# Kernel tuning notes

Hardware: AMD Instinct MI355X
Metric: run time of the kernel (lower is better)

The kernel has to match this reference:

```python
import jax, jax.numpy as jnp
import numpy as np
import math

B, H, N, D = 4, 16, 2048, 64
EPS = 1e-8


def setup_inputs() -> dict:
    key = jax.random.key(0)
    kq, kk, kv = jax.random.split(key, 3)
    Q = jax.random.normal(kq, (B, H, N, D), dtype=jnp.float32)
    K = jax.random.normal(kk, (B, H, N, D), dtype=jnp.float32)
    V = jax.random.normal(kv, (B, H, N, D), dtype=jnp.float32)
    # learnable per-head scale, init g0 = log2(N^2 - N)
    g0 = math.log2(N * N - N)
    qk_scale = jnp.full((H,), g0, dtype=jnp.float32)
    # causal mask, broadcast over (B, H)
    M = jnp.tril(jnp.ones((N, N), dtype=bool))
    return {"Q": Q, "K": K, "V": V, "qk_scale": qk_scale, "M": M}


def reference(Q, K, V, qk_scale, M):
    # L2-normalize Q and K along head dim (cosine attention)
    Q_hat = Q / (jnp.sqrt(jnp.sum(Q * Q, axis=-1, keepdims=True)) + EPS)
    K_hat = K / (jnp.sqrt(jnp.sum(K * K, axis=-1, keepdims=True)) + EPS)
    g = qk_scale[None, :, None, None]  # per-head learnable temperature
    scores = jnp.einsum('bhnd,bhmd->bhnm', Q_hat * g, K_hat)
    scores = jnp.where(M, scores, -jnp.inf)
    attn = jax.nn.softmax(scores, axis=-1)  # stable max-subtract softmax
    return jnp.einsum('bhnm,bhmd->bhnd', attn, V)
```

## Files before the change

kernel.cpp:

```cpp
#include <hip/hip_runtime.h>


#define BATCH 4
#define HEADS 16
#define SEQ   2048
#define DIM   64
#define EPS   1e-8f
#define LOG2E 1.44269504088896340736f

typedef short bf16x8 __attribute__((ext_vector_type(8)));
typedef short s16x4  __attribute__((ext_vector_type(4)));
typedef float fx16   __attribute__((ext_vector_type(16)));
typedef unsigned int u32x4 __attribute__((ext_vector_type(4)));

static __device__ __forceinline__ short f2bf(float x) {
    unsigned u = __float_as_uint(x);
    unsigned r = (u + 0x7fffu + ((u >> 16) & 1u)) >> 16;
    return (short)r;
}
static __device__ __forceinline__ unsigned cvt_pk(float lo, float hi) {
    unsigned r;
    asm("v_cvt_pk_bf16_f32 %0, %1, %2" : "=v"(r) : "v"(lo), "v"(hi));
    return r;
}
static __device__ __forceinline__ void gload_lds16(const short* g, short* l) {
    __builtin_amdgcn_global_load_lds(
        (const __attribute__((address_space(1))) void*)g,
        (__attribute__((address_space(3))) void*)l, 16, 0, 0);
}

#define TLDS 68

__global__ __launch_bounds__(256) void prep_kv(
    const float* __restrict__ K, const float* __restrict__ V,
    short* __restrict__ Kn, short* __restrict__ Vt)
{
    const int nt = blockIdx.x;
    const int bh = blockIdx.y;
    const int tid = threadIdx.x;

    const float* Kb = K + ((size_t)bh * SEQ + (size_t)nt * 64) * DIM;
    short* Kno = Kn + ((size_t)bh << 17) + (nt << 12);
    const int c4 = (tid & 15) * 4;
#pragma unroll
    for (int i = 0; i < 4; ++i) {
        const int r = i * 16 + (tid >> 4);
        float4 v = *(const float4*)(Kb + (size_t)r * DIM + c4);
        float ss = v.x * v.x + v.y * v.y + v.z * v.z + v.w * v.w;
        ss += __shfl_xor(ss, 1);
        ss += __shfl_xor(ss, 2);
        ss += __shfl_xor(ss, 4);
        ss += __shfl_xor(ss, 8);
        float s = 1.0f / (sqrtf(ss) + EPS);
        s16x4 o;
        o[0] = f2bf(v.x * s);
        o[1] = f2bf(v.y * s);
        o[2] = f2bf(v.z * s);
        o[3] = f2bf(v.w * s);
        *(s16x4*)(Kno + (r << 6) + (c4 ^ ((r & 7) << 3))) = o;
    }

    const float* Vb = V + ((size_t)bh * SEQ + (size_t)nt * 64) * DIM;
    short* Vo = Vt + ((size_t)bh << 17) + (nt << 12);
    __shared__ short lds[DIM * TLDS];
    const int cg = tid & 15;
    const int rr = tid >> 4;
#pragma unroll
    for (int i = 0; i < 4; ++i) {
        int n  = rr + i * 16;
        int d0 = cg * 4;
        float4 v = *(const float4*)(Vb + (size_t)n * DIM + d0);
        lds[(d0 + 0) * TLDS + n] = f2bf(v.x);
        lds[(d0 + 1) * TLDS + n] = f2bf(v.y);
        lds[(d0 + 2) * TLDS + n] = f2bf(v.z);
        lds[(d0 + 3) * TLDS + n] = f2bf(v.w);
    }
    __syncthreads();
#pragma unroll
    for (int i = 0; i < 4; ++i) {
        int d  = rr + i * 16;
        int nl = cg * 4;
        s16x4 o;
        o[0] = lds[d * TLDS + nl + 0];
        o[1] = lds[d * TLDS + nl + 1];
        o[2] = lds[d * TLDS + nl + 2];
        o[3] = lds[d * TLDS + nl + 3];
        *(s16x4*)(Vo + (d << 6) + (nl ^ ((d & 7) << 3))) = o;
    }
}

__global__ __launch_bounds__(512) void attn_fwd(
    const float* __restrict__ Q, const float* __restrict__ scale,
    const short* __restrict__ Kn, const short* __restrict__ Vt,
    float* __restrict__ out)
{
    const int lid = blockIdx.x;
    const int bh  = (lid & 7) * 8 + ((lid >> 3) & 7);
    const int qb  = 7 - (lid >> 6);
    const int tid = threadIdx.x;
    const int w   = tid >> 6;
    const int l   = tid & 63;
    const int lq  = l & 31;
    const int hi  = l >> 5;

    const short* Kb = Kn + ((size_t)bh << 17);
    const short* Vb = Vt + ((size_t)bh << 17);
    const float  g  = scale[bh & (HEADS - 1)];

    __shared__ __align__(16) short ldsK[4][64 * 64];
    __shared__ __align__(16) short ldsV[4][64 * 64];

    const int toff = tid * 8;

    const int wlo  = qb * 256 + w * 32;
    const int whi  = wlo + 31;
    const int qrow = wlo + lq;
    const int nkt  = 4 * qb + 4;

    gload_lds16(Kb + toff,        &ldsK[0][toff]);
    gload_lds16(Vb + toff,        &ldsV[0][toff]);
    gload_lds16(Kb + 4096 + toff, &ldsK[1][toff]);
    gload_lds16(Vb + 4096 + toff, &ldsV[1][toff]);

    const float* Qrow = Q + ((size_t)bh * SEQ + qrow) * DIM;
    float qv[4][8];
    float ss = 0.f;
#pragma unroll
    for (int c = 0; c < 4; ++c) {
        float4 a = *(const float4*)(Qrow + c * 16 + hi * 8);
        float4 b = *(const float4*)(Qrow + c * 16 + hi * 8 + 4);
        qv[c][0] = a.x; qv[c][1] = a.y; qv[c][2] = a.z; qv[c][3] = a.w;
        qv[c][4] = b.x; qv[c][5] = b.y; qv[c][6] = b.z; qv[c][7] = b.w;
#pragma unroll
        for (int jj = 0; jj < 8; ++jj) ss += qv[c][jj] * qv[c][jj];
    }
    ss += __shfl_xor(ss, 32);
    const float sc = g * LOG2E / (sqrtf(ss) + EPS);

    bf16x8 qbf[4];
#pragma unroll
    for (int c = 0; c < 4; ++c) {
        u32x4 wds;
#pragma unroll
        for (int m = 0; m < 4; ++m)
            wds[m] = cvt_pk(qv[c][2 * m] * sc, qv[c][2 * m + 1] * sc);
        qbf[c] = __builtin_bit_cast(bf16x8, wds);
    }

    fx16 oacc[2];
#pragma unroll
    for (int dt = 0; dt < 2; ++dt)
#pragma unroll
        for (int r = 0; r < 16; ++r) oacc[dt][r] = 0.f;
    float lsum = 0.f;

    int cur = 0;
    for (int kt = 0; kt < nkt; ++kt) {
        if (kt + 2 < nkt) {
            const int nb = (cur + 2) & 3;
            const short* gK = Kb + (size_t)(kt + 2) * 4096;
            const short* gV = Vb + (size_t)(kt + 2) * 4096;
            gload_lds16(gK + toff, &ldsK[nb][toff]);
            gload_lds16(gV + toff, &ldsV[nb][toff]);
            asm volatile("s_waitcnt vmcnt(4)" ::: "memory");
        } else if (kt + 1 < nkt) {
            asm volatile("s_waitcnt vmcnt(2)" ::: "memory");
        } else {
            asm volatile("s_waitcnt vmcnt(0)" ::: "memory");
        }
        __builtin_amdgcn_s_barrier();

        const int k0 = kt * 64;
        if (k0 <= whi) {
            const short* lk = ldsK[cur];
            const short* lv = ldsV[cur];

            fx16 sacc[2];
#pragma unroll
            for (int t = 0; t < 2; ++t)
#pragma unroll
                for (int r = 0; r < 16; ++r) sacc[t][r] = 0.f;

            bf16x8 kf[2][4];
#pragma unroll
            for (int t = 0; t < 2; ++t)
#pragma unroll
                for (int c = 0; c < 4; ++c) {
                    int r = t * 32 + lq;
                    kf[t][c] = *(const bf16x8*)
                        &lk[(r << 6) + ((c * 16 + hi * 8) ^ ((r & 7) << 3))];
                }
            __builtin_amdgcn_s_setprio(1);
#pragma unroll
            for (int c = 0; c < 4; ++c) {
                sacc[0] = __builtin_amdgcn_mfma_f32_32x32x16_bf16(kf[0][c], qbf[c], sacc[0], 0, 0, 0);
                sacc[1] = __builtin_amdgcn_mfma_f32_32x32x16_bf16(kf[1][c], qbf[c], sacc[1], 0, 0, 0);
            }
            __builtin_amdgcn_s_setprio(0);

            bf16x8 vf[2][4];
#pragma unroll
            for (int dt = 0; dt < 2; ++dt)
#pragma unroll
                for (int ks = 0; ks < 4; ++ks) {
                    int d = dt * 32 + lq;
                    vf[dt][ks] = *(const bf16x8*)
                        &lv[(d << 6) + ((ks * 16 + hi * 8) ^ ((d & 7) << 3))];
                }

            float pv[32];
#pragma unroll
            for (int t = 0; t < 2; ++t)
#pragma unroll
                for (int r = 0; r < 16; ++r) pv[t * 16 + r] = sacc[t][r];

            if (k0 + 63 > wlo) {
#pragma unroll
                for (int t = 0; t < 2; ++t)
#pragma unroll
                    for (int r = 0; r < 16; ++r) {
                        int key = k0 + 32 * t + (r & 3) + 8 * (r >> 2) + 4 * hi;
                        if (key > qrow) pv[t * 16 + r] = -3.0e38f;
                    }
            }

#pragma unroll
            for (int r = 0; r < 32; ++r)
                pv[r] = __builtin_amdgcn_exp2f(pv[r]);

            float ts[16];
#pragma unroll
            for (int r = 0; r < 16; ++r) ts[r] = pv[r] + pv[r + 16];
#pragma unroll
            for (int r = 0; r < 8; ++r) ts[r] += ts[r + 8];
#pragma unroll
            for (int r = 0; r < 4; ++r) ts[r] += ts[r + 4];
            float ps = (ts[0] + ts[1]) + (ts[2] + ts[3]);
            ps += __shfl_xor(ps, 32);
            lsum += ps;

            u32x4 paw[4];
#pragma unroll
            for (int ks = 0; ks < 4; ++ks) {
                const int t = ks >> 1;
                const int b0 = (ks & 1) * 8;
#pragma unroll
                for (int m = 0; m < 2; ++m) {
                    unsigned a = cvt_pk(pv[t * 16 + b0 + 2 * m], pv[t * 16 + b0 + 2 * m + 1]);
                    unsigned b = cvt_pk(pv[t * 16 + b0 + 2 * m + 4], pv[t * 16 + b0 + 2 * m + 5]);
                    asm("v_permlane32_swap_b32 %0, %1" : "+v"(a), "+v"(b));
                    paw[ks][m]     = a;
                    paw[ks][m + 2] = b;
                }
            }

            __builtin_amdgcn_s_setprio(1);
#pragma unroll
            for (int dt = 0; dt < 2; ++dt)
#pragma unroll
                for (int ks = 0; ks < 4; ++ks) {
                    bf16x8 pa = __builtin_bit_cast(bf16x8, paw[ks]);
                    oacc[dt] = __builtin_amdgcn_mfma_f32_32x32x16_bf16(vf[dt][ks], pa, oacc[dt], 0, 0, 0);
                }
            __builtin_amdgcn_s_setprio(0);
        }
        cur = (cur + 1) & 3;
    }

    float inv = 1.0f / lsum;
    size_t rb = ((size_t)bh * SEQ + (size_t)qrow) * DIM;
#pragma unroll
    for (int dt = 0; dt < 2; ++dt)
#pragma unroll
        for (int g4 = 0; g4 < 4; ++g4) {
            float4 o4;
            o4.x = oacc[dt][4 * g4 + 0] * inv;
            o4.y = oacc[dt][4 * g4 + 1] * inv;
            o4.z = oacc[dt][4 * g4 + 2] * inv;
            o4.w = oacc[dt][4 * g4 + 3] * inv;
            *(float4*)(out + rb + dt * 32 + 8 * g4 + 4 * hi) = o4;
        }
}

extern "C" void kernel_launch(void* const* d_in, const int* in_sizes, int n_in,
                              void* d_out, int out_size, void* d_ws, size_t ws_size,
                              hipStream_t stream)
{
    const float* Q  = (const float*)d_in[0];
    const float* K  = (const float*)d_in[1];
    const float* V  = (const float*)d_in[2];
    const float* qs = (const float*)d_in[3];
    float* out = (float*)d_out;

    const size_t nElem = (size_t)BATCH * HEADS * SEQ * DIM;
    short* Kn = (short*)d_ws;
    short* Vt = Kn + nElem;

    {
        dim3 grid(SEQ / 64, BATCH * HEADS);
        prep_kv<<<grid, 256, 0, stream>>>(K, V, Kn, Vt);
    }
    {
        attn_fwd<<<(SEQ / 256) * BATCH * HEADS, 512, 0, stream>>>(Q, qs, Kn, Vt, out);
    }
}
```

Before: 71.05 us.

## Software-pipeline QK^T of the next key tile with softmax of current

The key loop is restructured so that the QK^T MFMAs for tile kt+1 are issued while the exp2, row-sum and bf16 packing of tile kt run. Two score accumulator pairs are ping-ponged through a macro-unrolled loop of two tiles, and a prologue computes the first tile's scores. The prefetch wait tightens from vmcnt(4) to vmcnt(2), because the next tile must already be resident in LDS when its scores are computed early. The aim is to hide the MFMA latency behind VALU softmax work. The cost is higher register pressure from the extra accumulators, which may cut occupancy.

```diff
diff --git a/kernel.cpp b/kernel.cpp
--- a/kernel.cpp
+++ b/kernel.cpp
@@ -154,118 +154,119 @@
         for (int r = 0; r < 16; ++r) oacc[dt][r] = 0.f;
     float lsum = 0.f;
 
-    int cur = 0;
-    for (int kt = 0; kt < nkt; ++kt) {
-        if (kt + 2 < nkt) {
-            const int nb = (cur + 2) & 3;
-            const short* gK = Kb + (size_t)(kt + 2) * 4096;
-            const short* gV = Vb + (size_t)(kt + 2) * 4096;
-            gload_lds16(gK + toff, &ldsK[nb][toff]);
-            gload_lds16(gV + toff, &ldsV[nb][toff]);
-            asm volatile("s_waitcnt vmcnt(4)" ::: "memory");
-        } else if (kt + 1 < nkt) {
-            asm volatile("s_waitcnt vmcnt(2)" ::: "memory");
-        } else {
-            asm volatile("s_waitcnt vmcnt(0)" ::: "memory");
+    asm volatile("s_waitcnt vmcnt(2)" ::: "memory");
+    __builtin_amdgcn_s_barrier();
+
+    fx16 saccA0, saccA1, saccB0, saccB1;
+#pragma unroll
+    for (int r = 0; r < 16; ++r) { saccA0[r] = 0.f; saccA1[r] = 0.f; }
+    {
+        const short* lk = ldsK[0];
+#pragma unroll
+        for (int c = 0; c < 4; ++c) {
+            int r0 = lq, r1 = 32 + lq;
+            bf16x8 k0f = *(const bf16x8*)&lk[(r0 << 6) + ((c * 16 + hi * 8) ^ ((r0 & 7) << 3))];
+            bf16x8 k1f = *(const bf16x8*)&lk[(r1 << 6) + ((c * 16 + hi * 8) ^ ((r1 & 7) << 3))];
+            saccA0 = __builtin_amdgcn_mfma_f32_32x32x16_bf16(k0f, qbf[c], saccA0, 0, 0, 0);
+            saccA1 = __builtin_amdgcn_mfma_f32_32x32x16_bf16(k1f, qbf[c], saccA1, 0, 0, 0);
         }
-        __builtin_amdgcn_s_barrier();
-
-        const int k0 = kt * 64;
-        if (k0 <= whi) {
-            const short* lk = ldsK[cur];
-            const short* lv = ldsV[cur];
-
-            fx16 sacc[2];
-#pragma unroll
-            for (int t = 0; t < 2; ++t)
-#pragma unroll
-                for (int r = 0; r < 16; ++r) sacc[t][r] = 0.f;
-
-            bf16x8 kf[2][4];
-#pragma unroll
-            for (int t = 0; t < 2; ++t)
-#pragma unroll
-                for (int c = 0; c < 4; ++c) {
-                    int r = t * 32 + lq;
-                    kf[t][c] = *(const bf16x8*)
-                        &lk[(r << 6) + ((c * 16 + hi * 8) ^ ((r & 7) << 3))];
-                }
-            __builtin_amdgcn_s_setprio(1);
-#pragma unroll
-            for (int c = 0; c < 4; ++c) {
-                sacc[0] = __builtin_amdgcn_mfma_f32_32x32x16_bf16(kf[0][c], qbf[c], sacc[0], 0, 0, 0);
-                sacc[1] = __builtin_amdgcn_mfma_f32_32x32x16_bf16(kf[1][c], qbf[c], sacc[1], 0, 0, 0);
-            }
-            __builtin_amdgcn_s_setprio(0);
-
-            bf16x8 vf[2][4];
-#pragma unroll
-            for (int dt = 0; dt < 2; ++dt)
-#pragma unroll
-                for (int ks = 0; ks < 4; ++ks) {
-                    int d = dt * 32 + lq;
-                    vf[dt][ks] = *(const bf16x8*)
-                        &lv[(d << 6) + ((ks * 16 + hi * 8) ^ ((d & 7) << 3))];
-                }
-
-            float pv[32];
-#pragma unroll
-            for (int t = 0; t < 2; ++t)
-#pragma unroll
-                for (int r = 0; r < 16; ++r) pv[t * 16 + r] = sacc[t][r];
-
-            if (k0 + 63 > wlo) {
-#pragma unroll
-                for (int t = 0; t < 2; ++t)
-#pragma unroll
-                    for (int r = 0; r < 16; ++r) {
-                        int key = k0 + 32 * t + (r & 3) + 8 * (r >> 2) + 4 * hi;
-                        if (key > qrow) pv[t * 16 + r] = -3.0e38f;
-                    }
-            }
-
-#pragma unroll
-            for (int r = 0; r < 32; ++r)
-                pv[r] = __builtin_amdgcn_exp2f(pv[r]);
-
-            float ts[16];
-#pragma unroll
-            for (int r = 0; r < 16; ++r) ts[r] = pv[r] + pv[r + 16];
-#pragma unroll
-            for (int r = 0; r < 8; ++r) ts[r] += ts[r + 8];
-#pragma unroll
-            for (int r = 0; r < 4; ++r) ts[r] += ts[r + 4];
-            float ps = (ts[0] + ts[1]) + (ts[2] + ts[3]);
-            ps += __shfl_xor(ps, 32);
-            lsum += ps;
-
-            u32x4 paw[4];
-#pragma unroll
-            for (int ks = 0; ks < 4; ++ks) {
-                const int t = ks >> 1;
-                const int b0 = (ks & 1) * 8;
-#pragma unroll
-                for (int m = 0; m < 2; ++m) {
-                    unsigned a = cvt_pk(pv[t * 16 + b0 + 2 * m], pv[t * 16 + b0 + 2 * m + 1]);
-                    unsigned b = cvt_pk(pv[t * 16 + b0 + 2 * m + 4], pv[t * 16 + b0 + 2 * m + 5]);
-                    asm("v_permlane32_swap_b32 %0, %1" : "+v"(a), "+v"(b));
-                    paw[ks][m]     = a;
-                    paw[ks][m + 2] = b;
-                }
-            }
-
-            __builtin_amdgcn_s_setprio(1);
-#pragma unroll
-            for (int dt = 0; dt < 2; ++dt)
-#pragma unroll
-                for (int ks = 0; ks < 4; ++ks) {
-                    bf16x8 pa = __builtin_bit_cast(bf16x8, paw[ks]);
-                    oacc[dt] = __builtin_amdgcn_mfma_f32_32x32x16_bf16(vf[dt][ks], pa, oacc[dt], 0, 0, 0);
-                }
-            __builtin_amdgcn_s_setprio(0);
-        }
-        cur = (cur + 1) & 3;
-    }
+    }
+
+#define TILE_BODY(KT, SC0, SC1, SN0, SN1)                                    \
+    {                                                                        \
+        if ((KT) + 2 < nkt) {                                                \
+            const int nb = ((KT) + 2) & 3;                                   \
+            gload_lds16(Kb + (size_t)((KT) + 2) * 4096 + toff, &ldsK[nb][toff]); \
+            gload_lds16(Vb + (size_t)((KT) + 2) * 4096 + toff, &ldsV[nb][toff]); \
+            asm volatile("s_waitcnt vmcnt(2)" ::: "memory");                 \
+        } else {                                                             \
+            asm volatile("s_waitcnt vmcnt(0)" ::: "memory");                 \
+        }                                                                    \
+        __builtin_amdgcn_s_barrier();                                        \
+        const int k0 = (KT) * 64;                                            \
+        if (k0 <= whi) {                                                     \
+                              \
+            if (k0 + 63 > wlo) {                                             \
+                _Pragma("unroll")                                            \
+                for (int r = 0; r < 16; ++r) {                               \
+                    int key0 = k0 + (r & 3) + 8 * (r >> 2) + 4 * hi;         \
+                    if (key0 > qrow) SC0[r] = -3.0e38f;                      \
+                    if (key0 + 32 > qrow) SC1[r] = -3.0e38f;                 \
+                }                                                            \
+            }                                                                \
+                                                   \
+            _Pragma("unroll")                                                \
+            for (int r = 0; r < 16; ++r) {                                   \
+                SC0[r] = __builtin_amdgcn_exp2f(SC0[r]);                     \
+                SC1[r] = __builtin_amdgcn_exp2f(SC1[r]);                     \
+            }                                                                \
+                    \
+            if ((KT) + 1 < nkt) {                                            \
+                _Pragma("unroll")                                            \
+                for (int r = 0; r < 16; ++r) { SN0[r] = 0.f; SN1[r] = 0.f; } \
+                const short* lkn = ldsK[((KT) + 1) & 3];                     \
+                __builtin_amdgcn_s_setprio(1);                               \
+                _Pragma("unroll")                                            \
+                for (int c = 0; c < 4; ++c) {                                \
+                    int r0 = lq, r1 = 32 + lq;                               \
+                    bf16x8 k0f = *(const bf16x8*)&lkn[(r0 << 6) + ((c * 16 + hi * 8) ^ ((r0 & 7) << 3))]; \
+                    bf16x8 k1f = *(const bf16x8*)&lkn[(r1 << 6) + ((c * 16 + hi * 8) ^ ((r1 & 7) << 3))]; \
+                    SN0 = __builtin_amdgcn_mfma_f32_32x32x16_bf16(k0f, qbf[c], SN0, 0, 0, 0); \
+                    SN1 = __builtin_amdgcn_mfma_f32_32x32x16_bf16(k1f, qbf[c], SN1, 0, 0, 0); \
+                }                                                            \
+                __builtin_amdgcn_s_setprio(0);                               \
+            }                                                                \
+                                                        \
+            float ts[16];                                                    \
+            _Pragma("unroll")                                                \
+            for (int r = 0; r < 16; ++r) ts[r] = SC0[r] + SC1[r];            \
+            _Pragma("unroll")                                                \
+            for (int r = 0; r < 8; ++r) ts[r] += ts[r + 8];                  \
+            _Pragma("unroll")                                                \
+            for (int r = 0; r < 4; ++r) ts[r] += ts[r + 4];                  \
+            float ps = (ts[0] + ts[1]) + (ts[2] + ts[3]);                    \
+            ps += __shfl_xor(ps, 32);                                        \
+            lsum += ps;                                                      \
+                                                    \
+            u32x4 paw[4];                                                    \
+            _Pragma("unroll")                                                \
+            for (int ks = 0; ks < 4; ++ks) {                                 \
+                const int b0 = (ks & 1) * 8;                                 \
+                _Pragma("unroll")                                            \
+                for (int m = 0; m < 2; ++m) {                                \
+                    float xa0 = (ks < 2) ? SC0[b0 + 2 * m]     : SC1[b0 + 2 * m];     \
+                    float xa1 = (ks < 2) ? SC0[b0 + 2 * m + 1] : SC1[b0 + 2 * m + 1]; \
+                    float xb0 = (ks < 2) ? SC0[b0 + 2 * m + 4] : SC1[b0 + 2 * m + 4]; \
+                    float xb1 = (ks < 2) ? SC0[b0 + 2 * m + 5] : SC1[b0 + 2 * m + 5]; \
+                    unsigned a = cvt_pk(xa0, xa1);                           \
+                    unsigned b = cvt_pk(xb0, xb1);                           \
+                    asm("v_permlane32_swap_b32 %0, %1" : "+v"(a), "+v"(b));  \
+                    paw[ks][m]     = a;                                      \
+                    paw[ks][m + 2] = b;                                      \
+                }                                                            \
+            }                                                                \
+                                                           \
+            const short* lv = ldsV[(KT) & 3];                                \
+            __builtin_amdgcn_s_setprio(1);                                   \
+            _Pragma("unroll")                                                \
+            for (int dt = 0; dt < 2; ++dt) {                                 \
+                _Pragma("unroll")                                            \
+                for (int ks = 0; ks < 4; ++ks) {                             \
+                    int d = dt * 32 + lq;                                    \
+                    bf16x8 vf = *(const bf16x8*)&lv[(d << 6) + ((ks * 16 + hi * 8) ^ ((d & 7) << 3))]; \
+                    bf16x8 pa = __builtin_bit_cast(bf16x8, paw[ks]);         \
+                    oacc[dt] = __builtin_amdgcn_mfma_f32_32x32x16_bf16(vf, pa, oacc[dt], 0, 0, 0); \
+                }                                                            \
+            }                                                                \
+            __builtin_amdgcn_s_setprio(0);                                   \
+        }                                                                    \
+    }
+
+    for (int kt = 0; kt < nkt; kt += 2) {
+        TILE_BODY(kt,     saccA0, saccA1, saccB0, saccB1);
+        TILE_BODY(kt + 1, saccB0, saccB1, saccA0, saccA1);
+    }
+#undef TILE_BODY
 
     float inv = 1.0f / lsum;
     size_t rb = ((size_t)bh * SEQ + (size_t)qrow) * DIM;
```

New measurement: 76.03 us. +7.0%, slower.
